# Optimization experiments

Measured on AMD Instinct MI355X. Metric: run time of the kernel, lower is better.

Reference implementation:

```python
import jax, jax.numpy as jnp
import numpy as np

B = 32768; E = 9; RANK = 50; K = 2
N_ENT = 40943; N_REL = 22
LOSS_COEF = 0.01; NOISE_EPS = 0.01
EPS = float(np.finfo(np.float64).eps)


def setup_inputs():
    key = jax.random.key(0)
    ks = jax.random.split(key, 12)
    q0 = jax.random.randint(ks[0], (B,), 0, N_ENT)
    q1 = jax.random.randint(ks[1], (B,), 0, N_REL)
    q2 = jax.random.randint(ks[2], (B,), 0, N_ENT)
    queries = jnp.stack([q0, q1, q2], axis=1)
    t2 = jax.random.randint(ks[3], (B,), 0, N_ENT)
    these_queries = jnp.stack([q0, q1, t2], axis=1)
    D = E * RANK
    entity = jax.random.normal(ks[4], (N_ENT, D), jnp.float32) / D
    rel = jax.random.normal(ks[5], (N_REL, 2 * D), jnp.float32) / (2 * D)
    rel_diag = 2.0 * jax.random.uniform(ks[6], (N_REL, D), jnp.float32) - 1.0
    bh = jnp.zeros((N_ENT, 1), jnp.float32)
    bt = jnp.zeros((N_ENT, 1), jnp.float32)
    c_param = jnp.ones((N_REL, 1), jnp.float32)
    cnn_w = 0.1 * jax.random.normal(ks[7], (1, 1, 5, 5), jnp.float32)
    cnn_b = jnp.zeros((1,), jnp.float32)
    h2e_w = 0.05 * jax.random.normal(ks[8], (E, 128), jnp.float32)
    h2e_b = jnp.zeros((E,), jnp.float32)
    cnnn_w = 0.1 * jax.random.normal(ks[9], (1, 1, 5, 5), jnp.float32)
    cnnn_b = jnp.zeros((1,), jnp.float32)
    h2en_w = 0.05 * jax.random.normal(ks[10], (E, 128), jnp.float32)
    h2en_b = jnp.zeros((E,), jnp.float32)
    noise = jax.random.normal(ks[11], (B, E), jnp.float32)
    return {"queries": queries, "these_queries": these_queries, "entity": entity,
            "rel": rel, "rel_diag": rel_diag, "bh": bh, "bt": bt, "c_param": c_param,
            "cnn_w": cnn_w, "cnn_b": cnn_b, "h2e_w": h2e_w, "h2e_b": h2e_b,
            "cnnn_w": cnnn_w, "cnnn_b": cnnn_b, "h2en_w": h2en_w, "h2en_b": h2en_b,
            "noise": noise}


def _conv(x, w, b):
    # x: [B,1,27,50], w: [1,1,5,5], stride 3, VALID -> [B,1,8,16]
    y = jax.lax.conv_general_dilated(x, w, (3, 3), 'VALID',
                                     dimension_numbers=('NCHW', 'OIHW', 'NCHW'))
    return y + b.reshape(1, -1, 1, 1)


def _phi(z):
    # standard normal CDF
    return 0.5 * (1.0 + jax.lax.erf(z * 0.7071067811865476))


def _givens_rot(r, x):
    # r, x: [B,E,RANK]; rotate consecutive dim-pairs by normalized (cos,sin) from r
    shp = r.shape[:-1] + (RANK // 2, 2)
    r2 = r.reshape(shp); x2 = x.reshape(shp)
    nrm = jnp.maximum(jnp.linalg.norm(r2, axis=-1, keepdims=True), 1e-15)
    cs = r2 / nrm
    o0 = cs[..., 0] * x2[..., 0] - cs[..., 1] * x2[..., 1]
    o1 = cs[..., 1] * x2[..., 0] + cs[..., 0] * x2[..., 1]
    return jnp.stack([o0, o1], axis=-1).reshape(r.shape)


def _cv_squared(v):
    return jnp.var(v, ddof=1) / (jnp.mean(v) ** 2 + 1e-10)


def reference(queries, these_queries, entity, rel, rel_diag, bh, bt, c_param,
              cnn_w, cnn_b, h2e_w, h2e_b, cnnn_w, cnnn_b, h2en_w, h2en_b, noise):
    q0, q1 = queries[:, 0], queries[:, 1]
    t2 = these_queries[:, 2]
    head = entity[q0]                  # [B, E*RANK]
    rel_q = rel[q1]                    # [B, 2*E*RANK]
    rel_diag_q = rel_diag[q1]          # [B, E*RANK]
    c = jax.nn.softplus(c_param[q1])   # [B, 1]
    lhs_b = bh[q0]                     # [B, 1]
    rhs_b = bt[t2]                     # [B, 1]
    rhs_e = entity[t2]                 # [B, E*RANK]

    # ---- noisy top-k gating ----
    x = jnp.concatenate([head, rel_q], axis=-1).reshape(-1, 1, 3 * E, RANK)
    feat = _conv(x, cnn_w, cnn_b).reshape(-1, 128)
    clean = feat @ h2e_w.T + h2e_b                      # [B, E]
    feat_n = _conv(x, cnnn_w, cnnn_b).reshape(-1, 128)
    raw_std = feat_n @ h2en_w.T + h2en_b
    std = jax.nn.softplus(raw_std) + NOISE_EPS
    noisy = clean + noise * std                         # train=1

    top_logits, top_idx = jax.lax.top_k(noisy, K + 1)
    tk_logits = top_logits[:, :K]
    tk_idx = top_idx[:, :K]
    tk_gates = jax.nn.softmax(tk_logits, axis=-1)
    gates = jnp.zeros_like(noisy).at[jnp.arange(noisy.shape[0])[:, None], tk_idx].set(tk_gates)

    thr_in = top_logits[:, K:K + 1]
    thr_out = top_logits[:, K - 1:K]
    is_in = noisy > thr_in
    prob = jnp.where(is_in, _phi((clean - thr_in) / std), _phi((clean - thr_out) / std))
    load = prob.sum(0)
    importance = gates.sum(0)
    loss = LOSS_COEF * (_cv_squared(importance) + _cv_squared(load))

    # ---- experts, computed densely over [B, E, RANK] then masked-combined ----
    head_r = head.reshape(-1, E, RANK)
    rhs_r = rhs_e.reshape(-1, E, RANK)
    rel_r = rel_q.reshape(-1, E, 2 * RANK)
    rd_r = rel_diag_q.reshape(-1, E, RANK)
    lhs = _givens_rot(rd_r, head_r) + rel_r[..., :RANK]
    dist2 = jnp.sum((lhs - rhs_r) ** 2, axis=-1)        # [B, E]
    score = lhs_b + rhs_b - c * dist2                   # [B, E]

    # SparseDispatcher.combine with use_log_sum_exp=True, multiply_by_gates=False
    mask = gates > 0
    s = jnp.sum(jnp.where(mask, jnp.exp(score), 0.0), axis=1, keepdims=True)
    y = jnp.log(jnp.where(s == 0, EPS, s))              # [B, 1]
    return y, loss
```

## Files before the change

kernel.cpp:

```cpp
#include <hip/hip_runtime.h>
#include <math.h>

#define BATCH 32768
#define NE 9
#define RANK 50
#define DIM 450
#define REL_DIM 900
#define N_REL 22
#define EPSV 2.2204460492503131e-16f

__device__ __forceinline__ float softplusf(float x) {
    return (x > 20.f) ? x : log1pf(expf(x));
}
__device__ __forceinline__ float phif(float z) {
    return 0.5f * (1.f + erff(z * 0.70710678118654752f));
}

__global__ __launch_bounds__(64) void k_pre(
    const float* __restrict__ rel, const float* __restrict__ rel_diag,
    const float* __restrict__ c_param,
    const float* __restrict__ cnn_w, const float* __restrict__ cnn_b,
    const float* __restrict__ cnnn_w, const float* __restrict__ cnnn_b,
    const float* __restrict__ h2e_w, const float* __restrict__ h2en_w,
    float* __restrict__ cs_tab, float* __restrict__ pre_out, float* __restrict__ c_soft)
{
    const int r = blockIdx.x;
    const int l = threadIdx.x;
    __shared__ float rl[REL_DIM];
    __shared__ float fA[80], fB[80];

    const float* relp = rel + (size_t)r * REL_DIM;
    for (int i = l; i < REL_DIM; i += 64) rl[i] = relp[i];
    __syncthreads();

    const float cb0 = cnn_b[0], cb1 = cnnn_b[0];
    for (int idx = l; idx < 80; idx += 64) {
        int o = 48 + idx;
        int oh = o >> 4, ow = o & 15;
        const float* base = rl + (oh * 3 - 9) * RANK + ow * 3;
        float a0 = cb0, a1 = cb1;
#pragma unroll
        for (int i = 0; i < 5; ++i)
#pragma unroll
            for (int j = 0; j < 5; ++j) {
                float v = base[i * RANK + j];
                a0 = fmaf(v, cnn_w[i * 5 + j], a0);
                a1 = fmaf(v, cnnn_w[i * 5 + j], a1);
            }
        fA[idx] = a0; fB[idx] = a1;
    }
    __syncthreads();

    if (l < 18) {
        int e = (l < 9) ? l : (l - 9);
        const float* w = ((l < 9) ? (h2e_w + e * 128) : (h2en_w + e * 128)) + 48;
        const float* f = (l < 9) ? fA : fB;
        float acc = 0.f;
#pragma unroll 8
        for (int t = 0; t < 80; ++t) acc = fmaf(f[t], w[t], acc);
        pre_out[r * 18 + l] = acc;
    }
    if (l == 63) c_soft[r] = softplusf(c_param[r]);

    const float2* rd2 = (const float2*)(rel_diag + (size_t)r * DIM);
    float2* cs2 = (float2*)(cs_tab + (size_t)r * DIM);
    for (int u = l; u < 225; u += 64) {
        float2 v = rd2[u];
        float nrm = fmaxf(sqrtf(v.x * v.x + v.y * v.y), 1e-15f);
        cs2[u] = make_float2(v.x / nrm, v.y / nrm);
    }
}

__global__ __launch_bounds__(64) void k_main(
    const int* __restrict__ queries, const int* __restrict__ these_queries,
    const float* __restrict__ entity, const float* __restrict__ rel,
    const float* __restrict__ bh, const float* __restrict__ bt,
    const float* __restrict__ cnn_w, const float* __restrict__ cnn_b,
    const float* __restrict__ h2e_w, const float* __restrict__ h2e_b,
    const float* __restrict__ cnnn_w, const float* __restrict__ cnnn_b,
    const float* __restrict__ h2en_w, const float* __restrict__ h2en_b,
    const float* __restrict__ noise,
    const float* __restrict__ cs_tab, const float* __restrict__ pre_out,
    const float* __restrict__ c_soft,
    float* __restrict__ y_out, float* __restrict__ ws_rows)
{
    const int b = blockIdx.x;
    const int l = threadIdx.x;

    __shared__ __align__(16) float xs[552];
    __shared__ __align__(16) float ts[450];
    __shared__ __align__(16) float2 fs[51];
    __shared__ float clean_s[NE], stdv_s[NE], noisy_s[NE];
    __shared__ int   sidx[2];
    __shared__ float sg[2];
    __shared__ float sthr[2];

    const int q0 = queries[b * 3 + 0];
    const int q1 = queries[b * 3 + 1];
    const int t2 = these_queries[b * 3 + 2];

    const float2* hp2 = (const float2*)(entity + (size_t)q0 * DIM);
    const float2* tp2 = (const float2*)(entity + (size_t)t2 * DIM);
    const float2* rp2 = (const float2*)(rel + (size_t)q1 * REL_DIM);

    float2 h2[4], tt[4];
#pragma unroll
    for (int k = 0; k < 4; ++k) { int i = l + 64 * k; if (i < 225) h2[k] = hp2[i]; }
#pragma unroll
    for (int k = 0; k < 4; ++k) { int i = l + 64 * k; if (i < 225) tt[k] = tp2[i]; }
    float2 rr2 = make_float2(0.f, 0.f);
    if (l < 50) rr2 = rp2[l];
    float nz = 0.f;
    if (l < NE) nz = noise[(size_t)b * NE + l];
    float pre_v = 0.f;
    if (l < 18) pre_v = pre_out[q1 * 18 + l];

    float2* xs2 = (float2*)xs;
    float2* ts2 = (float2*)ts;
#pragma unroll
    for (int k = 0; k < 4; ++k) { int i = l + 64 * k; if (i < 225) xs2[i] = h2[k]; }
    if (l < 50) xs2[225 + l] = rr2;
    __syncthreads();

    if (l < 48) {
        int oh = l >> 4, ow = l & 15;
        const float* base = xs + (oh * 3) * RANK + ow * 3;
        float a0 = cnn_b[0], a1 = cnnn_b[0];
#pragma unroll
        for (int i = 0; i < 5; ++i)
#pragma unroll
            for (int j = 0; j < 5; ++j) {
                float v = base[i * RANK + j];
                a0 = fmaf(v, cnn_w[i * 5 + j], a0);
                a1 = fmaf(v, cnnn_w[i * 5 + j], a1);
            }
        fs[l + (l >> 4)] = make_float2(a0, a1);
    }
    __syncthreads();

    float acc = 0.f;
    if (l < 54) {
        int chunk = l / 18, j = l - chunk * 18;
        int e = (j < 9) ? j : (j - 9);
        const float* wrow = ((j < 9) ? (h2e_w + e * 128) : (h2en_w + e * 128)) + chunk * 16;
        int fbase = chunk * 17;
        if (j < 9) {
#pragma unroll
            for (int k = 0; k < 16; ++k) acc = fmaf(fs[fbase + k].x, wrow[k], acc);
        } else {
#pragma unroll
            for (int k = 0; k < 16; ++k) acc = fmaf(fs[fbase + k].y, wrow[k], acc);
        }
    }
    float pA = __shfl_down(acc, 18);
    float pB = __shfl_down(acc, 36);
    float tot = acc + pA + pB;
    if (l < 9)        clean_s[l]     = tot + pre_v + h2e_b[l];
    else if (l < 18)  stdv_s[l - 9]  = softplusf(tot + pre_v + h2en_b[l - 9]) + 0.01f;
    __syncthreads();
    if (l < NE) noisy_s[l] = fmaf(nz, stdv_s[l], clean_s[l]);

#pragma unroll
    for (int k = 0; k < 4; ++k) { int i = l + 64 * k; if (i < 225) ts2[i] = tt[k]; }
    __syncthreads();

    if (l == 0) {
        int i0 = -1, i1 = -1;
        float v0 = -__builtin_huge_valf(), v1 = v0, v2 = v0;
#pragma unroll
        for (int e = 0; e < NE; ++e) {
            float v = noisy_s[e];
            if (v > v0)      { v2 = v1; v1 = v0; i1 = i0; v0 = v; i0 = e; }
            else if (v > v1) { v2 = v1; v1 = v; i1 = e; }
            else if (v > v2) { v2 = v; }
        }
        float e1 = expf(v1 - v0);
        float inv = 1.f / (1.f + e1);
        sidx[0] = i0; sidx[1] = i1;
        sg[0] = inv; sg[1] = e1 * inv;
        sthr[0] = v2; sthr[1] = v1;
    }
    __syncthreads();

    float contrib = 0.f;
    bool act = (l < 25) || (l >= 32 && l < 57);
    if (act) {
        int sel = (l >= 32) ? 1 : 0;
        int p = l - 32 * sel;
        int e = sidx[sel];
        int u = e * 25 + p;
        float2 cs = *(const float2*)(cs_tab + (size_t)q1 * DIM + 2 * u);
        float2 rl = *(const float2*)(rel + (size_t)q1 * REL_DIM + e * 100 + 2 * p);
        float2 rh = ts2[u];
        float2 x  = xs2[u];
        float o0 = cs.x * x.x - cs.y * x.y + rl.x;
        float o1 = cs.y * x.x + cs.x * x.y + rl.y;
        float d0 = o0 - rh.x, d1 = o1 - rh.y;
        contrib = fmaf(d0, d0, d1 * d1);
    }

    if (l < NE) {
        float g = (l == sidx[0]) ? sg[0] : ((l == sidx[1]) ? sg[1] : 0.f);
        ws_rows[(size_t)b * 18 + l] = g;
    } else if (l < 18) {
        int e = l - 9;
        float thr_in = sthr[0], thr_out = sthr[1];
        float n = noisy_s[e];
        float thr = (n > thr_in) ? thr_in : thr_out;
        ws_rows[(size_t)b * 18 + 9 + e] = phif((clean_s[e] - thr) / stdv_s[e]);
    }

#pragma unroll
    for (int off = 16; off; off >>= 1) contrib += __shfl_xor(contrib, off);
    float d2b = __shfl(contrib, 32);
    if (l == 0) {
        float c = c_soft[q1];
        float base = bh[q0] + bt[t2];
        float s = expf(base - c * contrib) + expf(base - c * d2b);
        y_out[b] = logf((s == 0.f) ? EPSV : s);
    }
}

__global__ __launch_bounds__(64) void k_reduce(const float* __restrict__ ws_rows,
                                               float* __restrict__ partials)
{
    const int blk = blockIdx.x, t = threadIdx.x;
    float acc[18];
#pragma unroll
    for (int j = 0; j < 18; ++j) acc[j] = 0.f;
    const int r0 = blk * 128 + t * 2;
#pragma unroll
    for (int rr = 0; rr < 2; ++rr) {
        const float2* row = (const float2*)(ws_rows + (size_t)(r0 + rr) * 18);
#pragma unroll
        for (int j = 0; j < 9; ++j) {
            float2 v = row[j];
            acc[2 * j] += v.x; acc[2 * j + 1] += v.y;
        }
    }
#pragma unroll
    for (int j = 0; j < 18; ++j) {
        float v = acc[j];
        for (int off = 32; off; off >>= 1) v += __shfl_down(v, off);
        if (t == 0) partials[blk * 18 + j] = v;
    }
}

__global__ __launch_bounds__(64) void k_loss(const float* __restrict__ partials,
                                             float* __restrict__ out)
{
    __shared__ float sums[18];
    const int t = threadIdx.x;
    if (t < 18) {
        float s = 0.f;
        for (int p0 = 0; p0 < 256; p0 += 16) {
            float v[16];
#pragma unroll
            for (int k = 0; k < 16; ++k) v[k] = partials[(p0 + k) * 18 + t];
#pragma unroll
            for (int k = 0; k < 16; ++k) s += v[k];
        }
        sums[t] = s;
    }
    __syncthreads();
    if (t == 0) {
        float loss = 0.f;
#pragma unroll
        for (int part = 0; part < 2; ++part) {
            const float* v = sums + part * NE;
            float mean = 0.f;
            for (int i = 0; i < NE; ++i) mean += v[i];
            mean /= 9.f;
            float var = 0.f;
            for (int i = 0; i < NE; ++i) { float d = v[i] - mean; var += d * d; }
            var /= 8.f;
            loss += var / (mean * mean + 1e-10f);
        }
        out[BATCH] = 0.01f * loss;
    }
}

extern "C" void kernel_launch(void* const* d_in, const int* in_sizes, int n_in,
                              void* d_out, int out_size, void* d_ws, size_t ws_size,
                              hipStream_t stream)
{
    const int*   queries = (const int*)d_in[0];
    const int*   these   = (const int*)d_in[1];
    const float* entity  = (const float*)d_in[2];
    const float* rel     = (const float*)d_in[3];
    const float* rel_dg  = (const float*)d_in[4];
    const float* bh      = (const float*)d_in[5];
    const float* bt      = (const float*)d_in[6];
    const float* c_par   = (const float*)d_in[7];
    const float* cnn_w   = (const float*)d_in[8];
    const float* cnn_b   = (const float*)d_in[9];
    const float* h2e_w   = (const float*)d_in[10];
    const float* h2e_b   = (const float*)d_in[11];
    const float* cnnn_w  = (const float*)d_in[12];
    const float* cnnn_b  = (const float*)d_in[13];
    const float* h2en_w  = (const float*)d_in[14];
    const float* h2en_b  = (const float*)d_in[15];
    const float* noise   = (const float*)d_in[16];

    float* y  = (float*)d_out;
    float* ws = (float*)d_ws;
    float* ws_rows  = ws;
    float* partials = ws + (size_t)BATCH * 18;
    float* cs_tab   = partials + 256 * 18;
    float* pre_out  = cs_tab + N_REL * DIM;
    float* c_soft   = pre_out + N_REL * 18;

    k_pre<<<N_REL, 64, 0, stream>>>(rel, rel_dg, c_par, cnn_w, cnn_b, cnnn_w, cnnn_b,
                                    h2e_w, h2en_w, cs_tab, pre_out, c_soft);
    k_main<<<BATCH, 64, 0, stream>>>(queries, these, entity, rel, bh, bt,
                                     cnn_w, cnn_b, h2e_w, h2e_b, cnnn_w, cnnn_b,
                                     h2en_w, h2en_b, noise, cs_tab, pre_out, c_soft,
                                     y, ws_rows);
    k_reduce<<<256, 64, 0, stream>>>(ws_rows, partials);
    k_loss<<<1, 64, 0, stream>>>(partials, y);
}
```

Baseline: 185.6 us.

## Process four samples per wavefront with register prefetch and shuffle-based gating

```diff
diff --git a/kernel.cpp b/kernel.cpp
--- a/kernel.cpp
+++ b/kernel.cpp
@@ -8,6 +8,9 @@
 #define REL_DIM 900
 #define N_REL 22
 #define EPSV 2.2204460492503131e-16f
+#define SPB 4
+
+#define LANE_FENCE() asm volatile("" ::: "memory")
 
 __device__ __forceinline__ float softplusf(float x) {
     return (x > 20.f) ? x : log1pf(expf(x));
@@ -84,140 +87,147 @@
     const float* __restrict__ c_soft,
     float* __restrict__ y_out, float* __restrict__ ws_rows)
 {
-    const int b = blockIdx.x;
     const int l = threadIdx.x;
 
-    __shared__ __align__(16) float xs[552];
-    __shared__ __align__(16) float ts[450];
+    __shared__ __align__(16) float  xs[552];
     __shared__ __align__(16) float2 fs[51];
-    __shared__ float clean_s[NE], stdv_s[NE], noisy_s[NE];
-    __shared__ int   sidx[2];
-    __shared__ float sg[2];
-    __shared__ float sthr[2];
-
-    const int q0 = queries[b * 3 + 0];
-    const int q1 = queries[b * 3 + 1];
-    const int t2 = these_queries[b * 3 + 2];
-
-    const float2* hp2 = (const float2*)(entity + (size_t)q0 * DIM);
-    const float2* tp2 = (const float2*)(entity + (size_t)t2 * DIM);
-    const float2* rp2 = (const float2*)(rel + (size_t)q1 * REL_DIM);
-
-    float2 h2[4], tt[4];
-#pragma unroll
-    for (int k = 0; k < 4; ++k) { int i = l + 64 * k; if (i < 225) h2[k] = hp2[i]; }
-#pragma unroll
-    for (int k = 0; k < 4; ++k) { int i = l + 64 * k; if (i < 225) tt[k] = tp2[i]; }
+    float2* xs2 = (float2*)xs;
+
+    const int base = blockIdx.x * SPB;
+
+    int q0 = queries[base * 3 + 0];
+    int q1 = queries[base * 3 + 1];
+    int t2 = these_queries[base * 3 + 2];
+    float2 h2[4];
+    {
+        const float2* hp2 = (const float2*)(entity + (size_t)q0 * DIM);
+#pragma unroll
+        for (int k = 0; k < 4; ++k) { int i = l + 64 * k; if (i < 225) h2[k] = hp2[i]; }
+    }
     float2 rr2 = make_float2(0.f, 0.f);
-    if (l < 50) rr2 = rp2[l];
-    float nz = 0.f;
-    if (l < NE) nz = noise[(size_t)b * NE + l];
-    float pre_v = 0.f;
-    if (l < 18) pre_v = pre_out[q1 * 18 + l];
-
-    float2* xs2 = (float2*)xs;
-    float2* ts2 = (float2*)ts;
-#pragma unroll
-    for (int k = 0; k < 4; ++k) { int i = l + 64 * k; if (i < 225) xs2[i] = h2[k]; }
-    if (l < 50) xs2[225 + l] = rr2;
-    __syncthreads();
-
-    if (l < 48) {
-        int oh = l >> 4, ow = l & 15;
-        const float* base = xs + (oh * 3) * RANK + ow * 3;
-        float a0 = cnn_b[0], a1 = cnnn_b[0];
-#pragma unroll
-        for (int i = 0; i < 5; ++i)
-#pragma unroll
-            for (int j = 0; j < 5; ++j) {
-                float v = base[i * RANK + j];
-                a0 = fmaf(v, cnn_w[i * 5 + j], a0);
-                a1 = fmaf(v, cnnn_w[i * 5 + j], a1);
+    if (l < 50) rr2 = ((const float2*)(rel + (size_t)q1 * REL_DIM))[l];
+    float nz    = (l < NE) ? noise[(size_t)base * NE + l] : 0.f;
+    float pre_v = (l < 18) ? pre_out[q1 * 18 + l] : 0.f;
+    float bhv = bh[q0], btv = bt[t2], csv = c_soft[q1];
+
+#pragma unroll
+    for (int s = 0; s < SPB; ++s) {
+        const int b = base + s;
+        const int   cq1 = q1, ct2 = t2;
+        const float cnz = nz, cpre = pre_v, cbh = bhv, cbt = btv, ccs = csv;
+
+#pragma unroll
+        for (int k = 0; k < 4; ++k) { int i = l + 64 * k; if (i < 225) xs2[i] = h2[k]; }
+        if (l < 50) xs2[225 + l] = rr2;
+        LANE_FENCE();
+
+        if (s + 1 < SPB) {
+            const int nb = b + 1;
+            q0 = queries[nb * 3 + 0];
+            q1 = queries[nb * 3 + 1];
+            t2 = these_queries[nb * 3 + 2];
+            const float2* hp2 = (const float2*)(entity + (size_t)q0 * DIM);
+#pragma unroll
+            for (int k = 0; k < 4; ++k) { int i = l + 64 * k; if (i < 225) h2[k] = hp2[i]; }
+            rr2 = make_float2(0.f, 0.f);
+            if (l < 50) rr2 = ((const float2*)(rel + (size_t)q1 * REL_DIM))[l];
+            nz    = (l < NE) ? noise[(size_t)nb * NE + l] : 0.f;
+            pre_v = (l < 18) ? pre_out[q1 * 18 + l] : 0.f;
+            bhv = bh[q0]; btv = bt[t2]; csv = c_soft[q1];
+        }
+
+        if (l < 48) {
+            int oh = l >> 4, ow = l & 15;
+            const float* bp = xs + (oh * 3) * RANK + ow * 3;
+            float a0 = cnn_b[0], a1 = cnnn_b[0];
+#pragma unroll
+            for (int i = 0; i < 5; ++i)
+#pragma unroll
+                for (int j = 0; j < 5; ++j) {
+                    float v = bp[i * RANK + j];
+                    a0 = fmaf(v, cnn_w[i * 5 + j], a0);
+                    a1 = fmaf(v, cnnn_w[i * 5 + j], a1);
+                }
+            fs[l + (l >> 4)] = make_float2(a0, a1);
+        }
+        LANE_FENCE();
+
+        float acc = 0.f;
+        if (l < 54) {
+            int chunk = l / 18, j = l - chunk * 18;
+            int e = (j < 9) ? j : (j - 9);
+            const float* wrow = ((j < 9) ? (h2e_w + e * 128) : (h2en_w + e * 128)) + chunk * 16;
+            int fbase = chunk * 17;
+            if (j < 9) {
+#pragma unroll
+                for (int k = 0; k < 16; ++k) acc = fmaf(fs[fbase + k].x, wrow[k], acc);
+            } else {
+#pragma unroll
+                for (int k = 0; k < 16; ++k) acc = fmaf(fs[fbase + k].y, wrow[k], acc);
             }
-        fs[l + (l >> 4)] = make_float2(a0, a1);
-    }
-    __syncthreads();
-
-    float acc = 0.f;
-    if (l < 54) {
-        int chunk = l / 18, j = l - chunk * 18;
-        int e = (j < 9) ? j : (j - 9);
-        const float* wrow = ((j < 9) ? (h2e_w + e * 128) : (h2en_w + e * 128)) + chunk * 16;
-        int fbase = chunk * 17;
-        if (j < 9) {
-#pragma unroll
-            for (int k = 0; k < 16; ++k) acc = fmaf(fs[fbase + k].x, wrow[k], acc);
-        } else {
-#pragma unroll
-            for (int k = 0; k < 16; ++k) acc = fmaf(fs[fbase + k].y, wrow[k], acc);
-        }
-    }
-    float pA = __shfl_down(acc, 18);
-    float pB = __shfl_down(acc, 36);
-    float tot = acc + pA + pB;
-    if (l < 9)        clean_s[l]     = tot + pre_v + h2e_b[l];
-    else if (l < 18)  stdv_s[l - 9]  = softplusf(tot + pre_v + h2en_b[l - 9]) + 0.01f;
-    __syncthreads();
-    if (l < NE) noisy_s[l] = fmaf(nz, stdv_s[l], clean_s[l]);
-
-#pragma unroll
-    for (int k = 0; k < 4; ++k) { int i = l + 64 * k; if (i < 225) ts2[i] = tt[k]; }
-    __syncthreads();
-
-    if (l == 0) {
+        }
+        float pA = __shfl_down(acc, 18);
+        float pB = __shfl_down(acc, 36);
+        float tot = acc + pA + pB;
+
+        float myv = 0.f;
+        if (l < 9)       myv = tot + cpre + h2e_b[l];
+        else if (l < 18) myv = softplusf(tot + cpre + h2en_b[l - 9]) + 0.01f;
+        float sd = __shfl_down(myv, 9);
+        float nv = fmaf(cnz, sd, myv);
+
         int i0 = -1, i1 = -1;
         float v0 = -__builtin_huge_valf(), v1 = v0, v2 = v0;
 #pragma unroll
         for (int e = 0; e < NE; ++e) {
-            float v = noisy_s[e];
+            float v = __shfl(nv, e);
             if (v > v0)      { v2 = v1; v1 = v0; i1 = i0; v0 = v; i0 = e; }
             else if (v > v1) { v2 = v1; v1 = v; i1 = e; }
             else if (v > v2) { v2 = v; }
         }
         float e1 = expf(v1 - v0);
         float inv = 1.f / (1.f + e1);
-        sidx[0] = i0; sidx[1] = i1;
-        sg[0] = inv; sg[1] = e1 * inv;
-        sthr[0] = v2; sthr[1] = v1;
-    }
-    __syncthreads();
-
-    float contrib = 0.f;
-    bool act = (l < 25) || (l >= 32 && l < 57);
-    if (act) {
-        int sel = (l >= 32) ? 1 : 0;
-        int p = l - 32 * sel;
-        int e = sidx[sel];
-        int u = e * 25 + p;
-        float2 cs = *(const float2*)(cs_tab + (size_t)q1 * DIM + 2 * u);
-        float2 rl = *(const float2*)(rel + (size_t)q1 * REL_DIM + e * 100 + 2 * p);
-        float2 rh = ts2[u];
-        float2 x  = xs2[u];
-        float o0 = cs.x * x.x - cs.y * x.y + rl.x;
-        float o1 = cs.y * x.x + cs.x * x.y + rl.y;
-        float d0 = o0 - rh.x, d1 = o1 - rh.y;
-        contrib = fmaf(d0, d0, d1 * d1);
-    }
-
-    if (l < NE) {
-        float g = (l == sidx[0]) ? sg[0] : ((l == sidx[1]) ? sg[1] : 0.f);
-        ws_rows[(size_t)b * 18 + l] = g;
-    } else if (l < 18) {
-        int e = l - 9;
-        float thr_in = sthr[0], thr_out = sthr[1];
-        float n = noisy_s[e];
-        float thr = (n > thr_in) ? thr_in : thr_out;
-        ws_rows[(size_t)b * 18 + 9 + e] = phif((clean_s[e] - thr) / stdv_s[e]);
-    }
-
-#pragma unroll
-    for (int off = 16; off; off >>= 1) contrib += __shfl_xor(contrib, off);
-    float d2b = __shfl(contrib, 32);
-    if (l == 0) {
-        float c = c_soft[q1];
-        float base = bh[q0] + bt[t2];
-        float s = expf(base - c * contrib) + expf(base - c * d2b);
-        y_out[b] = logf((s == 0.f) ? EPSV : s);
+        float g0 = inv, g1 = e1 * inv;
+        float thr_in = v2, thr_out = v1;
+
+        int srcl = (l >= 9 && l < 18) ? (l - 9) : 0;
+        float cl_e = __shfl(myv, srcl);
+        float nv_e = __shfl(nv, srcl);
+
+        float contrib = 0.f;
+        bool act = (l < 25) || (l >= 32 && l < 57);
+        if (act) {
+            int sel = (l >= 32) ? 1 : 0;
+            int p = l - 32 * sel;
+            int e = sel ? i1 : i0;
+            int u = e * 25 + p;
+            float2 cs = *(const float2*)(cs_tab + (size_t)cq1 * DIM + 2 * u);
+            float2 rl = *(const float2*)(rel + (size_t)cq1 * REL_DIM + e * 100 + 2 * p);
+            float2 rh = *(const float2*)(entity + (size_t)ct2 * DIM + 2 * u);
+            float2 x  = xs2[u];
+            float o0 = cs.x * x.x - cs.y * x.y + rl.x;
+            float o1 = cs.y * x.x + cs.x * x.y + rl.y;
+            float d0 = o0 - rh.x, d1 = o1 - rh.y;
+            contrib = fmaf(d0, d0, d1 * d1);
+        }
+
+        if (l < NE) {
+            float g = (l == i0) ? g0 : ((l == i1) ? g1 : 0.f);
+            ws_rows[(size_t)b * 18 + l] = g;
+        } else if (l < 18) {
+            float thr = (nv_e > thr_in) ? thr_in : thr_out;
+            ws_rows[(size_t)b * 18 + l] = phif((cl_e - thr) / myv);
+        }
+
+#pragma unroll
+        for (int off = 16; off; off >>= 1) contrib += __shfl_xor(contrib, off);
+        float d2b = __shfl(contrib, 32);
+        if (l == 0) {
+            float bsum = cbh + cbt;
+            float sacc = expf(bsum - ccs * contrib) + expf(bsum - ccs * d2b);
+            y_out[b] = logf((sacc == 0.f) ? EPSV : sacc);
+        }
+        LANE_FENCE();
     }
 }
 
@@ -312,10 +322,10 @@
 
     k_pre<<<N_REL, 64, 0, stream>>>(rel, rel_dg, c_par, cnn_w, cnn_b, cnnn_w, cnnn_b,
                                     h2e_w, h2en_w, cs_tab, pre_out, c_soft);
-    k_main<<<BATCH, 64, 0, stream>>>(queries, these, entity, rel, bh, bt,
-                                     cnn_w, cnn_b, h2e_w, h2e_b, cnnn_w, cnnn_b,
-                                     h2en_w, h2en_b, noise, cs_tab, pre_out, c_soft,
-                                     y, ws_rows);
+    k_main<<<BATCH / SPB, 64, 0, stream>>>(queries, these, entity, rel, bh, bt,
+                                           cnn_w, cnn_b, h2e_w, h2e_b, cnnn_w, cnnn_b,
+                                           h2en_w, h2en_b, noise, cs_tab, pre_out, c_soft,
+                                           y, ws_rows);
     k_reduce<<<256, 64, 0, stream>>>(ws_rows, partials);
     k_loss<<<1, 64, 0, stream>>>(partials, y);
 }
```

Measured after the change: 193.7 us. 1.04x slower.
